# Optimization experiments

Measured on AMD Instinct MI355X. Metric: run time of the kernel, lower is better.

Reference implementation:

```python
import jax, jax.numpy as jnp
import numpy as np

DIM = 1024
NUM_HEADS = 16
HEAD_DIM = DIM // NUM_HEADS
SCALE = HEAD_DIM ** -0.5


def setup_inputs() -> dict:
    key = jax.random.key(0)
    ks = jax.random.split(key, 5)
    x = jax.random.normal(ks[0], (4, 1024, DIM), dtype=jnp.float32)
    w_qkv = jax.random.normal(ks[1], (DIM, 3 * DIM), dtype=jnp.float32) * (DIM ** -0.5)
    b_qkv = jnp.zeros((3 * DIM,), dtype=jnp.float32)
    w_proj = jax.random.normal(ks[2], (DIM, DIM), dtype=jnp.float32) * (DIM ** -0.5)
    b_proj = jnp.zeros((DIM,), dtype=jnp.float32)
    return {"x": x, "w_qkv": w_qkv, "b_qkv": b_qkv, "w_proj": w_proj, "b_proj": b_proj}


def reference(x, w_qkv, b_qkv, w_proj, b_proj):
    B, N, C = x.shape
    qkv = x @ w_qkv + b_qkv                                  # [B, N, 3C]
    qkv = qkv.reshape(B, N, 3, NUM_HEADS, HEAD_DIM)
    qkv = jnp.transpose(qkv, (2, 0, 3, 1, 4))                # [3, B, H, N, d]
    q, k, v = qkv[0] * SCALE, qkv[1], qkv[2]
    # attn scores in float32 (clamp to finfo range is a no-op after the cast)
    attn = jnp.einsum('bhnd,bhmd->bhnm', q, k).astype(jnp.float32)
    f32 = jnp.finfo(jnp.float32)
    attn = jnp.clip(attn, f32.min, f32.max)
    attn = jax.nn.softmax(attn, axis=-1)
    out = jnp.einsum('bhnm,bhmd->bhnd', attn, v)             # [B, H, N, d]
    out = jnp.transpose(out, (0, 2, 1, 3)).reshape(B, N, C)
    return out @ w_proj + b_proj
```

## Files before the change

kernel.cpp:

```cpp
#include <hip/hip_runtime.h>


typedef _Float16 half8 __attribute__((ext_vector_type(8)));
typedef _Float16 half4v __attribute__((ext_vector_type(4)));
typedef __fp16 fp16x2 __attribute__((ext_vector_type(2)));
typedef float floatx4 __attribute__((ext_vector_type(4)));

#define MFMA16(a, b, c) __builtin_amdgcn_mfma_f32_16x16x32_f16((a), (b), (c), 0, 0, 0)

static constexpr int DIM = 1024;
static constexpr int BATCH = 4;
static constexpr int SEQ = 1024;
static constexpr int NH = 16;
static constexpr int HD = 64;
static constexpr float SCALE = 0.125f;

__device__ static inline void gld16(_Float16* lds, const _Float16* g) {
    __builtin_amdgcn_global_load_lds(
        (const __attribute__((address_space(1))) void*)g,
        (__attribute__((address_space(3))) void*)lds, 16, 0, 0);
}

__global__ __launch_bounds__(256) void prep(const float* __restrict__ x,
                                            _Float16* __restrict__ xh,
                                            const float* __restrict__ wqkv,
                                            _Float16* __restrict__ wqkvT,
                                            const float* __restrict__ wproj,
                                            _Float16* __restrict__ wprojT) {
    __shared__ float tile[32][33];
    const int bid = blockIdx.x;
    const int tid = threadIdx.x;
    if (bid < 4096) {
        int i = (bid * 256 + tid) * 4;
        float4 v = *reinterpret_cast<const float4*>(x + i);
        half4v h;
        h[0] = (_Float16)v.x; h[1] = (_Float16)v.y;
        h[2] = (_Float16)v.z; h[3] = (_Float16)v.w;
        const int m = i >> 10, k = i & 1023;
        *reinterpret_cast<half4v*>(
            &xh[((size_t)(k >> 5) * 4096 + m) * 32 + (k & 31)]) = h;
        return;
    }
    const float* in;
    _Float16* out;
    int C, NN, bx, by;
    if (bid < 7168) {
        int b = bid - 4096;
        in = wqkv; out = wqkvT; C = 3072; NN = 3072;
        bx = b % 96; by = b / 96;
    } else {
        int b = bid - 7168;
        in = wproj; out = wprojT; C = 1024; NN = 1024;
        bx = b & 31; by = b >> 5;
    }
    const int c0 = bx * 32, r0 = by * 32;
    const int tx = tid & 31, ty = tid >> 5;
#pragma unroll
    for (int j = 0; j < 32; j += 8)
        tile[ty + j][tx] = in[(size_t)(r0 + ty + j) * C + (c0 + tx)];
    __syncthreads();
#pragma unroll
    for (int j = 0; j < 32; j += 8)
        out[((size_t)(r0 >> 5) * NN + (c0 + ty + j)) * 32 + tx] =
            (_Float16)tile[tx][ty + j];
}

template <int MODE>
__global__ __launch_bounds__(256, 2) void gemm_bt(const _Float16* __restrict__ A,
                                                  const _Float16* __restrict__ Bt,
                                                  const float* __restrict__ bias, int N,
                                                  float* __restrict__ outF,
                                                  _Float16* __restrict__ qbuf,
                                                  _Float16* __restrict__ kbuf,
                                                  _Float16* __restrict__ vtbuf) {
    constexpr int NT = 32;
    __shared__ _Float16 Ah[3 * 4096];
    __shared__ _Float16 Bh[3 * 4096];

    const int tid = threadIdx.x;
    const int wid = tid >> 6;
    const int lane = tid & 63;
    const int g = lane >> 4;
    const int ln = lane & 15;
    const int wr = wid >> 1, wc = wid & 1;
    const int m0 = blockIdx.y * 128;
    const int n0 = blockIdx.x * 128;
    const size_t PA = (size_t)4096 * 32;
    const size_t PB = (size_t)N * 32;
    const int woff = wid * 1024;
    const int lsw = (lane >> 2) * 32 + (((lane & 3) ^ ((lane >> 3) & 3)) * 8);
    const int gsw = (g ^ ((ln >> 1) & 3)) * 8;
    const _Float16* ga = A + (size_t)m0 * 32 + woff + lsw;
    const _Float16* gb = Bt + (size_t)n0 * 32 + woff + lsw;

    floatx4 acc[4][4];
#pragma unroll
    for (int i = 0; i < 4; ++i)
#pragma unroll
        for (int j = 0; j < 4; ++j) acc[i][j] = (floatx4){0.f, 0.f, 0.f, 0.f};

#pragma unroll
    for (int t = 0; t < 2; ++t) {
        gld16(&Ah[t * 4096 + woff], ga + t * PA);
        gld16(&Ah[t * 4096 + woff + 512], ga + t * PA + 512);
        gld16(&Bh[t * 4096 + woff], gb + t * PB);
        gld16(&Bh[t * 4096 + woff + 512], gb + t * PB + 512);
    }

    for (int kt = 0; kt < NT; ++kt) {
        if (kt < NT - 1) asm volatile("s_waitcnt vmcnt(4)" ::: "memory");
        else             asm volatile("s_waitcnt vmcnt(0)" ::: "memory");
        asm volatile("s_barrier" ::: "memory");
        if (kt < NT - 2) {
            const int pf = (kt + 2) % 3;
            const size_t ka = (size_t)(kt + 2) * PA;
            const size_t kb = (size_t)(kt + 2) * PB;
            gld16(&Ah[pf * 4096 + woff], ga + ka);
            gld16(&Ah[pf * 4096 + woff + 512], ga + ka + 512);
            gld16(&Bh[pf * 4096 + woff], gb + kb);
            gld16(&Bh[pf * 4096 + woff + 512], gb + kb + 512);
        }
        const _Float16* Ac = &Ah[(kt % 3) * 4096];
        const _Float16* Bc = &Bh[(kt % 3) * 4096];

        half8 af[4], bf[4];
#pragma unroll
        for (int i = 0; i < 4; ++i)
            af[i] = *reinterpret_cast<const half8*>(
                &Ac[(wr * 64 + i * 16 + ln) * 32 + gsw]);
#pragma unroll
        for (int j = 0; j < 4; ++j)
            bf[j] = *reinterpret_cast<const half8*>(
                &Bc[(wc * 64 + j * 16 + ln) * 32 + gsw]);
#pragma unroll
        for (int i = 0; i < 4; ++i)
#pragma unroll
            for (int j = 0; j < 4; ++j) acc[i][j] = MFMA16(af[i], bf[j], acc[i][j]);
    }

#pragma unroll
    for (int i = 0; i < 4; ++i) {
#pragma unroll
        for (int j = 0; j < 4; ++j) {
            const int n = n0 + wc * 64 + j * 16 + ln;
            const float bn = bias[n];
            const int mrow = m0 + wr * 64 + i * 16 + g * 4;
            if (MODE == 0) {
                const int which = n >> 10;
                const int rem = n & 1023;
                const int h = rem >> 6;
                const int dd = rem & 63;
                const int b = mrow >> 10, tok = mrow & 1023;
                const int bh = b * NH + h;
                if (which == 2) {
                    half4v pk;
#pragma unroll
                    for (int r = 0; r < 4; ++r) pk[r] = (_Float16)(acc[i][j][r] + bn);
                    *reinterpret_cast<half4v*>(
                        &vtbuf[((size_t)(bh * 32 + (tok >> 5)) * 64 + dd) * 32 +
                               (tok & 31)]) = pk;
                } else if (which == 1) {
#pragma unroll
                    for (int r = 0; r < 4; ++r)
                        kbuf[((size_t)(bh * 2 + (dd >> 5)) * SEQ + tok + r) * 32 +
                             (dd & 31)] = (_Float16)(acc[i][j][r] + bn);
                } else {
#pragma unroll
                    for (int r = 0; r < 4; ++r)
                        qbuf[(size_t)((bh << 10) + tok + r) * HD + dd] =
                            (_Float16)((acc[i][j][r] + bn) * SCALE);
                }
            } else {
#pragma unroll
                for (int r = 0; r < 4; ++r)
                    outF[(size_t)(mrow + r) * N + n] = acc[i][j][r] + bn;
            }
        }
    }
}

__global__ __launch_bounds__(256, 4) void flash_attn(const _Float16* __restrict__ qbuf,
                                                     const _Float16* __restrict__ kbuf,
                                                     const _Float16* __restrict__ vtbuf,
                                                     _Float16* __restrict__ attn_out) {
    __shared__ _Float16 Klds[2 * 4096];
    __shared__ _Float16 Vlds[2 * 4096];

    const int tid = threadIdx.x;
    const int wid = tid >> 6;
    const int lane = tid & 63;
    const int g = lane >> 4;
    const int ln = lane & 15;
    const int bh = blockIdx.x;
    const int qbase = blockIdx.y * 64 + wid * 16;
    const _Float16* qg = qbuf + ((size_t)bh << 10) * HD;
    const _Float16* kg = kbuf + (size_t)bh * (2 * SEQ * 32);
    const _Float16* vg = vtbuf + (size_t)bh * (32 * 64 * 32);

    const int woff = wid * 512;
    const int lsw = (lane >> 2) * 32 + (((lane & 3) ^ ((lane >> 3) & 3)) * 8);
    const int gsw = (g ^ ((ln >> 1) & 3)) * 8;
    const int sl0 = ((lane >> 4) & 1) * 32 + ln;
    const bool hi32 = (lane & 32) != 0;

    half8 qf[2];
#pragma unroll
    for (int f = 0; f < 2; ++f)
        qf[f] = *reinterpret_cast<const half8*>(
            qg + (size_t)(qbase + ln) * HD + f * 32 + g * 8);

    floatx4 o[4];
#pragma unroll
    for (int t = 0; t < 4; ++t) o[t] = (floatx4){0.f, 0.f, 0.f, 0.f};
    float l_lane = 0.f;

    constexpr int NT = SEQ / 64;
#pragma unroll
    for (int f = 0; f < 2; ++f) {
        gld16(&Klds[f * 2048 + woff], kg + (size_t)f * (SEQ * 32) + woff + lsw);
        gld16(&Vlds[f * 2048 + woff], vg + (size_t)f * 2048 + woff + lsw);
    }

    for (int kt = 0; kt < NT; ++kt) {
        asm volatile("s_waitcnt vmcnt(0)" ::: "memory");
        asm volatile("s_barrier" ::: "memory");
        const int cur = kt & 1;
        if (kt < NT - 1) {
            const int nb = cur ^ 1;
#pragma unroll
            for (int f = 0; f < 2; ++f) {
                gld16(&Klds[nb * 4096 + f * 2048 + woff],
                      kg + (size_t)f * (SEQ * 32) + (kt + 1) * 2048 + woff + lsw);
                gld16(&Vlds[nb * 4096 + f * 2048 + woff],
                      vg + (size_t)(2 * (kt + 1) + f) * 2048 + woff + lsw);
            }
        }
        const _Float16* Kb = &Klds[cur * 4096];
        const _Float16* Vb = &Vlds[cur * 4096];

        half8 kf[4][2], vf[4][2];
#pragma unroll
        for (int c = 0; c < 4; ++c)
#pragma unroll
            for (int f = 0; f < 2; ++f) {
                kf[c][f] = *reinterpret_cast<const half8*>(
                    &Kb[f * 2048 + (c * 16 + ln) * 32 + gsw]);
                vf[c][f] = *reinterpret_cast<const half8*>(
                    &Vb[f * 2048 + (c * 16 + ln) * 32 + gsw]);
            }

        floatx4 st[4];
#pragma unroll
        for (int c = 0; c < 4; ++c) {
            floatx4 z = (floatx4){0.f, 0.f, 0.f, 0.f};
            z = MFMA16(kf[c][0], qf[0], z);
            z = MFMA16(kf[c][1], qf[1], z);
            st[c] = z;
        }

        int pk[4][2];
#pragma unroll
        for (int c = 0; c < 4; ++c) {
            float p0 = __expf(st[c][0]);
            float p1 = __expf(st[c][1]);
            float p2 = __expf(st[c][2]);
            float p3 = __expf(st[c][3]);
            l_lane += (p0 + p1) + (p2 + p3);
            union { fp16x2 h; int i; } u0, u1;
            u0.h = __builtin_amdgcn_cvt_pkrtz(p0, p1);
            u1.h = __builtin_amdgcn_cvt_pkrtz(p2, p3);
            pk[c][0] = u0.i;
            pk[c][1] = u1.i;
        }

#pragma unroll
        for (int H = 0; H < 2; ++H) {
            int a0 = __shfl(pk[2 * H][0], sl0), b0 = __shfl(pk[2 * H + 1][0], sl0);
            int a1 = __shfl(pk[2 * H][1], sl0), b1 = __shfl(pk[2 * H + 1][1], sl0);
            int a2 = __shfl(pk[2 * H][0], sl0 + 16), b2 = __shfl(pk[2 * H + 1][0], sl0 + 16);
            int a3 = __shfl(pk[2 * H][1], sl0 + 16), b3 = __shfl(pk[2 * H + 1][1], sl0 + 16);
            union { int i[4]; half8 h; } ua;
            ua.i[0] = hi32 ? b0 : a0;
            ua.i[1] = hi32 ? b1 : a1;
            ua.i[2] = hi32 ? b2 : a2;
            ua.i[3] = hi32 ? b3 : a3;
#pragma unroll
            for (int t = 0; t < 4; ++t) o[t] = MFMA16(ua.h, vf[t][H], o[t]);
        }
    }

    l_lane += __shfl_xor(l_lane, 16);
    l_lane += __shfl_xor(l_lane, 32);

    const int b = bh >> 4, h = bh & 15;
#pragma unroll
    for (int r = 0; r < 4; ++r) {
        const float inv = 1.0f / __shfl(l_lane, g * 4 + r);
        const int tok = qbase + g * 4 + r;
#pragma unroll
        for (int t = 0; t < 4; ++t)
            attn_out[((size_t)(h * 2 + (t >> 1)) * 4096 + (b * SEQ + tok)) * 32 +
                     (t & 1) * 16 + ln] = (_Float16)(o[t][r] * inv);
    }
}

extern "C" void kernel_launch(void* const* d_in, const int* in_sizes, int n_in,
                              void* d_out, int out_size, void* d_ws, size_t ws_size,
                              hipStream_t stream) {
    const float* x = (const float*)d_in[0];
    const float* wqkv = (const float*)d_in[1];
    const float* bqkv = (const float*)d_in[2];
    const float* wproj = (const float*)d_in[3];
    const float* bproj = (const float*)d_in[4];
    float* out = (float*)d_out;

    char* ws = (char*)d_ws;
    _Float16* xh     = (_Float16*)(ws);
    _Float16* wqkvT  = (_Float16*)(ws + (8ull << 20));
    _Float16* qbuf   = (_Float16*)(ws + (14ull << 20));
    _Float16* kbuf   = (_Float16*)(ws + (22ull << 20));
    _Float16* vtbuf  = (_Float16*)(ws + (30ull << 20));
    _Float16* wprojT = (_Float16*)(ws + (38ull << 20));
    _Float16* attn   = xh;

    prep<<<8192, 256, 0, stream>>>(x, xh, wqkv, wqkvT, wproj, wprojT);
    gemm_bt<0><<<dim3(24, 32), 256, 0, stream>>>(xh, wqkvT, bqkv, 3 * DIM, nullptr,
                                                 qbuf, kbuf, vtbuf);
    flash_attn<<<dim3(BATCH * NH, SEQ / 64), 256, 0, stream>>>(qbuf, kbuf, vtbuf, attn);
    gemm_bt<1><<<dim3(8, 32), 256, 0, stream>>>(attn, wprojT, bproj, DIM, out,
                                                nullptr, nullptr, nullptr);
}
```

Measured before the change: 177.2 us.

## Give each wave private LDS tiles to remove block barriers in GEMM

The GEMM main loop now has each wave load only its own 64-row A and 64-column B slices into a per-wave double-buffered LDS region, so it waits only on its own vmcnt and drops the block-wide s_barrier. The shared 3-stage ring, in which the four waves cooperatively loaded 128x32 A and B tiles, is replaced. In exchange, each A and B slice is now loaded by two waves, doubling global/L2 traffic, and LDS use rises to 64KB per block. The launch_bounds minimum-occupancy hint of 2 is removed, which may lower occupancy.

```diff
diff --git a/kernel.cpp b/kernel.cpp
--- a/kernel.cpp
+++ b/kernel.cpp
@@ -66,16 +66,15 @@
 }
 
 template <int MODE>
-__global__ __launch_bounds__(256, 2) void gemm_bt(const _Float16* __restrict__ A,
-                                                  const _Float16* __restrict__ Bt,
-                                                  const float* __restrict__ bias, int N,
-                                                  float* __restrict__ outF,
-                                                  _Float16* __restrict__ qbuf,
-                                                  _Float16* __restrict__ kbuf,
-                                                  _Float16* __restrict__ vtbuf) {
+__global__ __launch_bounds__(256) void gemm_bt(const _Float16* __restrict__ A,
+                                               const _Float16* __restrict__ Bt,
+                                               const float* __restrict__ bias, int N,
+                                               float* __restrict__ outF,
+                                               _Float16* __restrict__ qbuf,
+                                               _Float16* __restrict__ kbuf,
+                                               _Float16* __restrict__ vtbuf) {
     constexpr int NT = 32;
-    __shared__ _Float16 Ah[3 * 4096];
-    __shared__ _Float16 Bh[3 * 4096];
+    __shared__ _Float16 S[4][2][4096];
 
     const int tid = threadIdx.x;
     const int wid = tid >> 6;
@@ -87,11 +86,11 @@
     const int n0 = blockIdx.x * 128;
     const size_t PA = (size_t)4096 * 32;
     const size_t PB = (size_t)N * 32;
-    const int woff = wid * 1024;
     const int lsw = (lane >> 2) * 32 + (((lane & 3) ^ ((lane >> 3) & 3)) * 8);
     const int gsw = (g ^ ((ln >> 1) & 3)) * 8;
-    const _Float16* ga = A + (size_t)m0 * 32 + woff + lsw;
-    const _Float16* gb = Bt + (size_t)n0 * 32 + woff + lsw;
+    const _Float16* ga = A + ((size_t)(m0 + wr * 64)) * 32 + lsw;
+    const _Float16* gb = Bt + ((size_t)(n0 + wc * 64)) * 32 + lsw;
+    _Float16* Sw = &S[wid][0][0];
 
     floatx4 acc[4][4];
 #pragma unroll
@@ -100,38 +99,35 @@
         for (int j = 0; j < 4; ++j) acc[i][j] = (floatx4){0.f, 0.f, 0.f, 0.f};
 
 #pragma unroll
-    for (int t = 0; t < 2; ++t) {
-        gld16(&Ah[t * 4096 + woff], ga + t * PA);
-        gld16(&Ah[t * 4096 + woff + 512], ga + t * PA + 512);
-        gld16(&Bh[t * 4096 + woff], gb + t * PB);
-        gld16(&Bh[t * 4096 + woff + 512], gb + t * PB + 512);
+    for (int c = 0; c < 4; ++c) {
+        gld16(Sw + c * 512, ga + c * 512);
+        gld16(Sw + 2048 + c * 512, gb + c * 512);
     }
 
     for (int kt = 0; kt < NT; ++kt) {
-        if (kt < NT - 1) asm volatile("s_waitcnt vmcnt(4)" ::: "memory");
-        else             asm volatile("s_waitcnt vmcnt(0)" ::: "memory");
-        asm volatile("s_barrier" ::: "memory");
-        if (kt < NT - 2) {
-            const int pf = (kt + 2) % 3;
-            const size_t ka = (size_t)(kt + 2) * PA;
-            const size_t kb = (size_t)(kt + 2) * PB;
-            gld16(&Ah[pf * 4096 + woff], ga + ka);
-            gld16(&Ah[pf * 4096 + woff + 512], ga + ka + 512);
-            gld16(&Bh[pf * 4096 + woff], gb + kb);
-            gld16(&Bh[pf * 4096 + woff + 512], gb + kb + 512);
-        }
-        const _Float16* Ac = &Ah[(kt % 3) * 4096];
-        const _Float16* Bc = &Bh[(kt % 3) * 4096];
+        const int cur = kt & 1;
+        if (kt < NT - 1) {
+            const size_t ka = (size_t)(kt + 1) * PA;
+            const size_t kb = (size_t)(kt + 1) * PB;
+            _Float16* Sn = Sw + (cur ^ 1) * 4096;
+#pragma unroll
+            for (int c = 0; c < 4; ++c) {
+                gld16(Sn + c * 512, ga + ka + c * 512);
+                gld16(Sn + 2048 + c * 512, gb + kb + c * 512);
+            }
+            asm volatile("s_waitcnt vmcnt(8)" ::: "memory");
+        } else {
+            asm volatile("s_waitcnt vmcnt(0)" ::: "memory");
+        }
+        const _Float16* Sc = Sw + cur * 4096;
 
         half8 af[4], bf[4];
 #pragma unroll
         for (int i = 0; i < 4; ++i)
-            af[i] = *reinterpret_cast<const half8*>(
-                &Ac[(wr * 64 + i * 16 + ln) * 32 + gsw]);
+            af[i] = *reinterpret_cast<const half8*>(&Sc[(i * 16 + ln) * 32 + gsw]);
 #pragma unroll
         for (int j = 0; j < 4; ++j)
-            bf[j] = *reinterpret_cast<const half8*>(
-                &Bc[(wc * 64 + j * 16 + ln) * 32 + gsw]);
+            bf[j] = *reinterpret_cast<const half8*>(&Sc[2048 + (j * 16 + ln) * 32 + gsw]);
 #pragma unroll
         for (int i = 0; i < 4; ++i)
 #pragma unroll
```

After: 176.8 us. No clear change (-0.2%).
